# Kernel tuning notes

Hardware: AMD Instinct MI355X
Metric: run time of the kernel (lower is better)

Reference implementation:

```python
import jax, jax.numpy as jnp
from jax import lax
import numpy as np

B, C_IN, H, W = 32, 3, 256, 256
EMB_DIM, NUM_EMB = 64, 512
COMMIT = 0.25
DN = ('NCHW', 'OIHW', 'NCHW')


def conv2d(x, w, b, stride, pad):
    y = lax.conv_general_dilated(x, w, (stride, stride), [(pad, pad), (pad, pad)],
                                 dimension_numbers=DN)
    return y + b[None, :, None, None]


def conv_transpose2d(x, w, b, stride, pad):
    # torch ConvTranspose2d weight layout: (in_ch, out_ch, kh, kw)
    # equivalent: regular conv with spatially flipped, (in,out)-swapped kernel,
    # lhs_dilation=stride, padding = k - 1 - pad on each side.
    k = w.shape[2]
    w_conv = jnp.flip(w, (2, 3)).transpose(1, 0, 2, 3)  # -> OIHW
    p = k - 1 - pad
    y = lax.conv_general_dilated(x, w_conv, (1, 1), [(p, p), (p, p)],
                                 lhs_dilation=(stride, stride), dimension_numbers=DN)
    return y + b[None, :, None, None]


def setup_inputs() -> dict:
    key = jax.random.key(0)
    ks = jax.random.split(key, 8)

    def rn(k, shape):
        fan_in = int(np.prod(shape[1:]))
        return jax.random.normal(k, shape, jnp.float32) / np.float32(np.sqrt(fan_in))

    return {
        "x": jax.random.normal(ks[0], (B, C_IN, H, W), jnp.float32),
        "e1_w": rn(ks[1], (32, C_IN, 4, 4)), "e1_b": jnp.zeros((32,), jnp.float32),
        "e2_w": rn(ks[2], (EMB_DIM, 32, 4, 4)), "e2_b": jnp.zeros((EMB_DIM,), jnp.float32),
        "emb": jax.random.uniform(ks[3], (NUM_EMB, EMB_DIM), jnp.float32,
                                  -1.0 / NUM_EMB, 1.0 / NUM_EMB),
        # decoder ConvTranspose weights in torch (in, out, k, k) layout
        "d1_w": rn(ks[4], (EMB_DIM, 64, 4, 4)), "d1_b": jnp.zeros((64,), jnp.float32),
        "d2_w": rn(ks[5], (64, 32, 4, 4)), "d2_b": jnp.zeros((32,), jnp.float32),
        "d3_w": rn(ks[6], (C_IN, 32, 3, 3)), "d3_b": jnp.zeros((C_IN,), jnp.float32),
    }


def vq(z, emb):
    Bz, Cz, Hz, Wz = z.shape
    flat = z.transpose(0, 2, 3, 1).reshape(-1, Cz)  # (B*H*W, C), NHWC order
    # squared euclidean distances; argmin identical to cdist argmin
    d2 = (jnp.sum(flat * flat, axis=1, keepdims=True)
          - 2.0 * flat @ emb.T
          + jnp.sum(emb * emb, axis=1))  # (N, K)
    idx = jnp.argmin(d2, axis=1)
    q_flat = emb[idx]  # gather == one-hot matmul in original
    # FAITHFUL to torch: .view(x.shape) reinterprets NHWC-ordered rows as NCHW
    quantized = q_flat.reshape(z.shape)
    loss = (COMMIT * jnp.mean((lax.stop_gradient(quantized) - z) ** 2)
            + jnp.mean((quantized - lax.stop_gradient(z)) ** 2))
    q_st = z + lax.stop_gradient(quantized - z)  # straight-through
    return q_st, loss, idx.reshape(Bz, Hz, Wz)


def reference(x, e1_w, e1_b, e2_w, e2_b, emb, d1_w, d1_b, d2_w, d2_b, d3_w, d3_b):
    z = jax.nn.relu(conv2d(x, e1_w, e1_b, 2, 1))
    z = jax.nn.relu(conv2d(z, e2_w, e2_b, 2, 1))
    q_st, vq_loss, _ = vq(z, emb)
    h = jax.nn.relu(conv_transpose2d(q_st, d1_w, d1_b, 2, 1))
    h = jax.nn.relu(conv_transpose2d(h, d2_w, d2_b, 2, 1))
    recon = jax.nn.sigmoid(conv2d(h, d3_w, d3_b, 1, 1))
    return recon, vq_loss, q_st
```

## Files before the change

### kernel.cpp

```cpp
#include <hip/hip_runtime.h>
#include <math.h>

#define BB    32
#define C_IN  3
#define H0    256
#define W0    256
#define C1    32
#define H1    128
#define W1    128
#define C2    64
#define H2    64
#define W2    64
#define HW2   (H2*W2)
#define N_EMB 512
#define E_DIM 64
#define NZ    (BB*C2*HW2)
#define NPX   (BB*HW2)

typedef unsigned short u16;
typedef unsigned int   uint;
typedef __attribute__((ext_vector_type(8))) short short8;
typedef __attribute__((ext_vector_type(4))) float f32x4;

__device__ inline u16 f2bf(float f) {
    uint u = __builtin_bit_cast(uint, f);
    u += 0x7FFF + ((u >> 16) & 1);
    return (u16)(u >> 16);
}
__device__ inline float bf2f(u16 h) {
    uint u = (uint)h << 16;
    return __builtin_bit_cast(float, u);
}
__device__ inline f32x4 mfma16(short8 a, short8 b, f32x4 c) {
    return __builtin_amdgcn_mfma_f32_16x16x32_bf16(a, b, c, 0, 0, 0);
}
template<int RS>
__device__ inline int swz(int off) { return off ^ (((off >> RS) & 7) << 4); }

template<int C, int HP, int WP, int H, int W>
__global__ __launch_bounds__(256) void border_zero(u16* buf, int nimg) {
    int t = blockIdx.x * 256 + threadIdx.x;
    if (t >= nimg * HP * WP) return;
    int x = t % WP, y = (t / WP) % HP;
    if (y >= 1 && y < 1 + H && x >= 1 && x < 1 + W) return;
    uint4 z4; z4.x = 0; z4.y = 0; z4.z = 0; z4.w = 0;
    uint4* p = (uint4*)(buf + (size_t)t * C);
    #pragma unroll
    for (int i = 0; i < C / 8; ++i) p[i] = z4;
}

template<int CI, int CO>
__global__ __launch_bounds__(256) void wt_deconv(const float* __restrict__ w,
        u16* __restrict__ wb) {
    int i = blockIdx.x * 256 + threadIdx.x;
    if (i >= 4 * CO * 4 * CI) return;
    int ic  = i % CI;
    int t   = (i / CI) & 3;
    int oc  = (i / (CI * 4)) % CO;
    int cls = i / (CI * 4 * CO);
    int py = cls >> 1, px = cls & 1, ty = t >> 1, tx = t & 1;
    int ky = py ? (ty ? 0 : 2) : (ty ? 3 : 1);
    int kx = px ? (tx ? 0 : 2) : (tx ? 3 : 1);
    wb[i] = f2bf(w[(((size_t)ic * CO + oc) * 4 + ky) * 4 + kx]);
}

__global__ __launch_bounds__(256) void wt_conv2(const float* __restrict__ w,
        u16* __restrict__ wb) {
    int i = blockIdx.x * 256 + threadIdx.x;
    if (i >= 64 * 512) return;
    int ic = i & 31;
    int k  = (i >> 5) & 15;
    int oc = i >> 9;
    wb[i] = f2bf(w[(size_t)(oc * 32 + ic) * 16 + k]);
}

__global__ __launch_bounds__(256) void wt_conv3(const float* __restrict__ w,
        u16* __restrict__ wk) {
    int i = blockIdx.x * 256 + threadIdx.x;
    if (i >= 16 * 288) return;
    int ic = i & 31;
    int k  = (i / 32) % 9;
    int oc = i / 288;
    float hi = 0.f, lo = 0.f;
    if (oc < 3) {
        float v = w[(size_t)(oc * 32 + ic) * 9 + k];
        hi = bf2f(f2bf(v));
        lo = v - hi;
    }
    wk[i]            = f2bf(hi);
    wk[i + 16 * 288] = f2bf(lo);
}

__global__ __launch_bounds__(256) void wt_emb(const float* __restrict__ emb,
        u16* __restrict__ ehi, u16* __restrict__ elo) {
    int i = blockIdx.x * 256 + threadIdx.x;
    float v = emb[i];
    u16 h = f2bf(v);
    ehi[i] = h;
    elo[i] = f2bf(v - bf2f(h));
}

__global__ __launch_bounds__(256) void conv1_kernel(const float* __restrict__ x,
        const float* __restrict__ w, const float* __restrict__ bias,
        u16* __restrict__ out) {
    int t = blockIdx.x * 256 + threadIdx.x;
    int ox = t & (W1 - 1);
    int oy = (t >> 7) & (H1 - 1);
    int b  = t >> 14;
    const float* xb = x + (size_t)b * (C_IN * H0 * W0);
    float v[48];
    #pragma unroll
    for (int ic = 0; ic < 3; ++ic)
        #pragma unroll
        for (int dy = 0; dy < 4; ++dy) {
            int iy = oy * 2 - 1 + dy;
            #pragma unroll
            for (int dx = 0; dx < 4; ++dx) {
                int ix = ox * 2 - 1 + dx;
                float val = 0.f;
                if ((unsigned)iy < H0 && (unsigned)ix < W0)
                    val = xb[((size_t)ic * H0 + iy) * W0 + ix];
                v[(ic * 4 + dy) * 4 + dx] = val;
            }
        }
    u16 h[32];
    #pragma unroll
    for (int oc = 0; oc < C1; ++oc) {
        float a = bias[oc];
        #pragma unroll
        for (int k = 0; k < 48; ++k) a = fmaf(v[k], w[oc * 48 + k], a);
        h[oc] = f2bf(fmaxf(a, 0.f));
    }
    uint4* dst = (uint4*)(out + ((size_t)(b * 131 + oy + 1) * 131 + ox + 1) * 32);
    #pragma unroll
    for (int i = 0; i < 4; ++i) {
        uint4 u;
        u.x = (uint)h[i*8+0] | ((uint)h[i*8+1] << 16);
        u.y = (uint)h[i*8+2] | ((uint)h[i*8+3] << 16);
        u.z = (uint)h[i*8+4] | ((uint)h[i*8+5] << 16);
        u.w = (uint)h[i*8+6] | ((uint)h[i*8+7] << 16);
        dst[i] = u;
    }
}

__global__ __launch_bounds__(256) void conv2_mfma(const u16* __restrict__ z1p,
        const u16* __restrict__ wb, const float* __restrict__ bias,
        float* __restrict__ z) {
    __shared__ u16 wlds[32 * 512];
    int xcd = blockIdx.x & 7;
    int oh  = (blockIdx.x >> 3) & 1;
    int bx  = (blockIdx.x >> 4) * 8 + xcd;
    for (int j = threadIdx.x; j < 2048; j += 256) {
        int u = j * 8;
        int byteoff = swz<10>(u * 2);
        *(uint4*)((char*)wlds + byteoff) =
            *(const uint4*)(wb + (size_t)(oh * 32) * 512 + u);
    }
    __syncthreads();
    int wid = threadIdx.x >> 6, lane = threadIdx.x & 63;
    int m0 = bx * 128 + wid * 32;
    int b  = m0 >> 12;
    int y  = (m0 >> 6) & 63;
    int x0 = m0 & 63;
    int l15 = lane & 15, lk = lane >> 4;
    f32x4 acc[2][2] = {};
    int xA = x0 + l15, xB = x0 + 16 + l15;
    for (int ks = 0; ks < 16; ++ks) {
        int dy = ks >> 2, dx = ks & 3;
        int rb = (b * 131 + 2 * y + dy) * 131;
        short8 fbA = *(const short8*)(z1p + ((size_t)(rb + 2 * xA + dx)) * 32 + lk * 8);
        short8 fbB = *(const short8*)(z1p + ((size_t)(rb + 2 * xB + dx)) * 32 + lk * 8);
        #pragma unroll
        for (int f = 0; f < 2; ++f) {
            int byteoff = swz<10>((f * 16 + l15) * 1024 + ks * 64 + lk * 16);
            short8 fa = *(const short8*)((const char*)wlds + byteoff);
            acc[0][f] = mfma16(fa, fbA, acc[0][f]);
            acc[1][f] = mfma16(fa, fbB, acc[1][f]);
        }
    }
    #pragma unroll
    for (int p = 0; p < 2; ++p) {
        int pix = m0 + p * 16 + l15;
        #pragma unroll
        for (int f = 0; f < 2; ++f) {
            int oc0 = oh * 32 + f * 16 + lk * 4;
            float4 bi = *(const float4*)(bias + oc0);
            float4 r;
            r.x = fmaxf(acc[p][f][0] + bi.x, 0.f);
            r.y = fmaxf(acc[p][f][1] + bi.y, 0.f);
            r.z = fmaxf(acc[p][f][2] + bi.z, 0.f);
            r.w = fmaxf(acc[p][f][3] + bi.w, 0.f);
            *(float4*)(z + (size_t)pix * 64 + oc0) = r;
        }
    }
}

__global__ void e2_kernel(const float* __restrict__ emb, float* __restrict__ e2) {
    int e = blockIdx.x * 64 + threadIdx.x;
    float s = 0.f;
    #pragma unroll
    for (int c = 0; c < E_DIM; ++c) {
        float v = emb[(size_t)e * E_DIM + c];
        s = fmaf(v, v, s);
    }
    e2[e] = s;
}

__global__ __launch_bounds__(256) void vq_mfma(const float* __restrict__ zf,
        const u16* __restrict__ ehi, const u16* __restrict__ elo,
        const float* __restrict__ e2, const float* __restrict__ emb,
        float* __restrict__ q, u16* __restrict__ dq) {
    int wid = threadIdx.x >> 6, lane = threadIdx.x & 63;
    int l15 = lane & 15, lk = lane >> 4;
    int m0 = (blockIdx.x * 4 + wid) * 32;
    short8 zh[2][2], zl[2][2];
    #pragma unroll
    for (int h = 0; h < 2; ++h) {
        int px = m0 + h * 16 + l15;
        const float4* zp = (const float4*)(zf + (size_t)px * 64);
        #pragma unroll
        for (int ks = 0; ks < 2; ++ks) {
            short8 hh, ll;
            #pragma unroll
            for (int j2 = 0; j2 < 2; ++j2) {
                float4 v4 = zp[ks * 8 + lk * 2 + j2];
                float vv[4] = {v4.x, v4.y, v4.z, v4.w};
                #pragma unroll
                for (int j = 0; j < 4; ++j) {
                    u16 hb = f2bf(vv[j]);
                    hh[j2 * 4 + j] = (short)hb;
                    ll[j2 * 4 + j] = (short)f2bf(vv[j] - bf2f(hb));
                }
            }
            zh[h][ks] = hh;
            zl[h][ks] = ll;
        }
    }
    float bs[2] = {3.4e38f, 3.4e38f};
    int   bi[2] = {0, 0};
    for (int tile = 0; tile < 32; ++tile) {
        short8 fh[2], fl[2];
        #pragma unroll
        for (int ks = 0; ks < 2; ++ks) {
            fh[ks] = *(const short8*)(ehi + (size_t)(tile * 16 + l15) * 64 + ks * 32 + lk * 8);
            fl[ks] = *(const short8*)(elo + (size_t)(tile * 16 + l15) * 64 + ks * 32 + lk * 8);
        }
        float4 e2v = *(const float4*)(e2 + tile * 16 + lk * 4);
        float ee[4] = {e2v.x, e2v.y, e2v.z, e2v.w};
        #pragma unroll
        for (int h = 0; h < 2; ++h) {
            f32x4 acc = {};
            #pragma unroll
            for (int ks = 0; ks < 2; ++ks) {
                acc = mfma16(fh[ks], zh[h][ks], acc);
                acc = mfma16(fl[ks], zh[h][ks], acc);
                acc = mfma16(fh[ks], zl[h][ks], acc);
            }
            #pragma unroll
            for (int r = 0; r < 4; ++r) {
                float sc = ee[r] - 2.f * acc[r];
                int ei = tile * 16 + lk * 4 + r;
                if (sc < bs[h]) { bs[h] = sc; bi[h] = ei; }
            }
        }
    }
    #pragma unroll
    for (int h = 0; h < 2; ++h) {
        #pragma unroll
        for (int off = 16; off < 64; off <<= 1) {
            float s2 = __shfl_xor(bs[h], off, 64);
            int   i2 = __shfl_xor(bi[h], off, 64);
            if (s2 < bs[h] || (s2 == bs[h] && i2 < bi[h])) { bs[h] = s2; bi[h] = i2; }
        }
    }
    #pragma unroll
    for (int h = 0; h < 2; ++h) {
        for (int p = 0; p < 16; ++p) {
            int idx = __shfl(bi[h], p, 64);
            int px  = m0 + h * 16 + p;
            float val = emb[(size_t)idx * 64 + lane];
            q[(size_t)px * 64 + lane] = val;
            int xx = px & 63, yy = (px >> 6) & 63, bb = px >> 12;
            dq[((size_t)(bb * 66 + yy + 1) * 66 + xx + 1) * 64 + lane] = f2bf(val);
        }
    }
}

__global__ __launch_bounds__(256) void loss_tr(const float* __restrict__ q,
        const float* __restrict__ z, float* __restrict__ part) {
    __shared__ float zt[64 * 65];
    int bh = blockIdx.x;
    size_t zbase = (size_t)bh * 4096;
    for (int j = threadIdx.x; j < 4096; j += 256) {
        int w = j >> 6, c = j & 63;
        zt[w * 65 + c] = z[zbase + j];
    }
    __syncthreads();
    int b = bh >> 6, h = bh & 63;
    int w = threadIdx.x & 63;
    float s = 0.f;
    #pragma unroll
    for (int k = 0; k < 16; ++k) {
        int cc = (threadIdx.x >> 6) + k * 4;
        float qv = q[(size_t)b * 262144 + (size_t)cc * 4096 + h * 64 + w];
        float d = qv - zt[w * 65 + cc];
        s = fmaf(d, d, s);
    }
    #pragma unroll
    for (int off = 32; off; off >>= 1) s += __shfl_down(s, off, 64);
    __shared__ float red[4];
    int lane = threadIdx.x & 63, wid = threadIdx.x >> 6;
    if (lane == 0) red[wid] = s;
    __syncthreads();
    if (threadIdx.x == 0) part[blockIdx.x] = (red[0] + red[1]) + (red[2] + red[3]);
}

__global__ __launch_bounds__(256) void loss_final(const float* __restrict__ part,
        float* __restrict__ loss, float scale) {
    float s = 0.f;
    for (int i = threadIdx.x; i < 2048; i += 256) s += part[i];
    #pragma unroll
    for (int off = 32; off; off >>= 1) s += __shfl_down(s, off, 64);
    __shared__ float red[4];
    int lane = threadIdx.x & 63, wid = threadIdx.x >> 6;
    if (lane == 0) red[wid] = s;
    __syncthreads();
    if (threadIdx.x == 0)
        *loss = ((red[0] + red[1]) + (red[2] + red[3])) * scale;
}

template<int CO, int NOC, int PT, int HI, int WI, int NYB>
__global__ __launch_bounds__(256) void deconv_lds(const u16* __restrict__ in,
        const u16* __restrict__ wb, const float* __restrict__ bias,
        u16* __restrict__ out) {
    constexpr int HPI = HI + 2, WPI = WI + 2;
    constexpr int HPO = 2 * HI + 2, WPO = 2 * WI + 2;
    constexpr int NF = NOC / 16;
    constexpr int NW16 = 2 * NOC * 256;
    constexpr int LOG2NYB = (NYB == 4) ? 2 : 1;
    __shared__ u16 wlds[NW16];
    int xcd = blockIdx.x & 7;
    int byv = (blockIdx.x >> 3) & (NYB - 1);
    int bx  = (blockIdx.x >> (3 + LOG2NYB)) * 8 + xcd;
    int py = byv & 1;
    int oh = byv >> 1;
    int oc_base = oh * NOC;
    for (int j = threadIdx.x; j < NW16 / 8; j += 256) {
        int u = j * 8;
        int clsl = u / (NOC * 256);
        int rem = u - clsl * (NOC * 256);
        int byteoff = swz<9>(u * 2);
        *(uint4*)((char*)wlds + byteoff) = *(const uint4*)(wb
            + ((size_t)((py * 2 + clsl) * CO + oc_base)) * 256 + rem);
    }
    __syncthreads();
    int sy = py ? 1 : -1;
    int wid = threadIdx.x >> 6, lane = threadIdx.x & 63;
    int m0 = bx * (PT * 64) + wid * (PT * 16);
    int b = m0 / (HI * WI);
    int rem0 = m0 % (HI * WI);
    int y = rem0 / WI, x0 = rem0 % WI;
    int l15 = lane & 15, lk = lane >> 4;

    short8 fbuf[2][3][2][PT];
    #pragma unroll
    for (int idy = 0; idy < 2; ++idy) {
        int dy = idy ? sy : 0;
        int rb = (b * HPI + y + dy + 1) * WPI;
        #pragma unroll
        for (int idx = 0; idx < 3; ++idx)
            #pragma unroll
            for (int ks = 0; ks < 2; ++ks)
                #pragma unroll
                for (int p = 0; p < PT; ++p)
                    fbuf[idy][idx][ks][p] = *(const short8*)(in
                        + (size_t)(rb + x0 + p * 16 + l15 + idx) * 64
                        + ks * 32 + lk * 8);
    }

    f32x4 acc[PT][2][NF] = {};
    #pragma unroll
    for (int idy = 0; idy < 2; ++idy)
        #pragma unroll
        for (int idx = 0; idx < 3; ++idx) {
            int dx = idx - 1;
            #pragma unroll
            for (int ks = 0; ks < 2; ++ks)
                #pragma unroll
                for (int pxc = 0; pxc < 2; ++pxc) {
                    int sx = pxc ? 1 : -1;
                    if (!(dx == 0 || dx == sx)) continue;
                    int t = 2 * (idy != 0) + (dx != 0);
                    #pragma unroll
                    for (int f = 0; f < NF; ++f) {
                        int row = pxc * NOC + f * 16 + l15;
                        int byteoff = swz<9>(row * 512 + (t * 2 + ks) * 64 + lk * 16);
                        short8 fa = *(const short8*)((const char*)wlds + byteoff);
                        #pragma unroll
                        for (int p = 0; p < PT; ++p)
                            acc[p][pxc][f] = mfma16(fa, fbuf[idy][idx][ks][p],
                                                    acc[p][pxc][f]);
                    }
                }
        }

    #pragma unroll
    for (int p = 0; p < PT; ++p) {
        int x = x0 + p * 16 + l15;
        #pragma unroll
        for (int pxc = 0; pxc < 2; ++pxc) {
            int oy = 2 * y + py + 1, ox = 2 * x + pxc + 1;
            size_t po = ((size_t)(b * HPO + oy) * WPO + ox) * CO;
            #pragma unroll
            for (int f = 0; f < NF; ++f) {
                int oc0 = oc_base + f * 16 + lk * 4;
                float4 bi = *(const float4*)(bias + oc0);
                float r0 = fmaxf(acc[p][pxc][f][0] + bi.x, 0.f);
                float r1 = fmaxf(acc[p][pxc][f][1] + bi.y, 0.f);
                float r2 = fmaxf(acc[p][pxc][f][2] + bi.z, 0.f);
                float r3 = fmaxf(acc[p][pxc][f][3] + bi.w, 0.f);
                uint2 uu;
                uu.x = (uint)f2bf(r0) | ((uint)f2bf(r1) << 16);
                uu.y = (uint)f2bf(r2) | ((uint)f2bf(r3) << 16);
                *(uint2*)(out + po + oc0) = uu;
            }
        }
    }
}

__global__ __launch_bounds__(512) void deconv2_stage(const u16* __restrict__ in,
        const u16* __restrict__ wb, const float* __restrict__ bias,
        u16* __restrict__ out) {
    __shared__ u16 wlds[2 * 32 * 256];
    __shared__ u16 ilds[2 * 130 * 64];
    int xcd = blockIdx.x & 7;
    int py  = (blockIdx.x >> 3) & 1;
    int bx  = (blockIdx.x >> 4) * 8 + xcd;
    int b = bx >> 7;
    int y = bx & 127;
    int sy = py ? 1 : -1;
    for (int j = threadIdx.x; j < 2048; j += 512) {
        int u = j * 8;
        int clsl = u >> 13;
        int rem = u & 8191;
        *(uint4*)((char*)wlds + swz<9>(u * 2)) = *(const uint4*)(wb
            + ((size_t)(py * 2 + clsl) * 32) * 256 + rem);
    }
    int rowg0 = (b * 130 + y + 1) * 130;
    int rowg1 = (b * 130 + y + sy + 1) * 130;
    for (int j = threadIdx.x; j < 2080; j += 512) {
        int row = (j >= 1040);
        int rem = j - row * 1040;
        int px = rem >> 3, c16 = rem & 7;
        int rg = row ? rowg1 : rowg0;
        uint4 v = *(const uint4*)(in + (size_t)(rg + px) * 64 + c16 * 8);
        int lbyte = (j * 16) ^ ((px & 7) << 4);
        *(uint4*)((char*)ilds + lbyte) = v;
    }
    __syncthreads();

    int wid = threadIdx.x >> 6, lane = threadIdx.x & 63;
    int l15 = lane & 15, lk = lane >> 4;
    int xw = wid * 16;
    f32x4 acc[2][2] = {};
    #pragma unroll
    for (int idy = 0; idy < 2; ++idy)
        #pragma unroll
        for (int idx = 0; idx < 3; ++idx) {
            int dx = idx - 1;
            #pragma unroll
            for (int ks = 0; ks < 2; ++ks) {
                int pxl = xw + l15 + idx;
                int lbyte = ((idy * 130 + pxl) * 128 + ks * 64 + lk * 16)
                            ^ ((pxl & 7) << 4);
                short8 fb = *(const short8*)((const char*)ilds + lbyte);
                #pragma unroll
                for (int pxc = 0; pxc < 2; ++pxc) {
                    int sx = pxc ? 1 : -1;
                    if (!(dx == 0 || dx == sx)) continue;
                    int t = 2 * (idy != 0) + (dx != 0);
                    #pragma unroll
                    for (int f = 0; f < 2; ++f) {
                        int row = pxc * 32 + f * 16 + l15;
                        int byteoff = swz<9>(row * 512 + (t * 2 + ks) * 64 + lk * 16);
                        short8 fa = *(const short8*)((const char*)wlds + byteoff);
                        acc[pxc][f] = mfma16(fa, fb, acc[pxc][f]);
                    }
                }
            }
        }

    int x = xw + l15;
    #pragma unroll
    for (int pxc = 0; pxc < 2; ++pxc) {
        int oy = 2 * y + py + 1, ox = 2 * x + pxc + 1;
        size_t po = ((size_t)(b * 258 + oy) * 258 + ox) * 32;
        #pragma unroll
        for (int f = 0; f < 2; ++f) {
            int oc0 = f * 16 + lk * 4;
            float4 bi = *(const float4*)(bias + oc0);
            float r0 = fmaxf(acc[pxc][f][0] + bi.x, 0.f);
            float r1 = fmaxf(acc[pxc][f][1] + bi.y, 0.f);
            float r2 = fmaxf(acc[pxc][f][2] + bi.z, 0.f);
            float r3 = fmaxf(acc[pxc][f][3] + bi.w, 0.f);
            uint2 uu;
            uu.x = (uint)f2bf(r0) | ((uint)f2bf(r1) << 16);
            uu.y = (uint)f2bf(r2) | ((uint)f2bf(r3) << 16);
            *(uint2*)(out + po + oc0) = uu;
        }
    }
}

__global__ __launch_bounds__(256) void conv3_mfma(const u16* __restrict__ in,
        const u16* __restrict__ wk, const float* __restrict__ bias,
        float* __restrict__ out) {
    __shared__ u16 walds[16 * 288 * 2];
    for (int j = threadIdx.x; j < 1152; j += 256) {
        int u = j * 8;
        *(uint4*)((char*)walds + swz<9>(u * 2)) = *(const uint4*)(wk + u);
    }
    __syncthreads();
    int wid = threadIdx.x >> 6, lane = threadIdx.x & 63;
    int m0 = (blockIdx.x * 4 + wid) * 16;
    int b   = m0 >> 16;
    int rem = m0 & 65535;
    int y   = rem >> 8;
    int x0  = rem & 255;
    int l15 = lane & 15, lk = lane >> 4;
    short8 fb[3][3];
    #pragma unroll
    for (int dy = 0; dy < 3; ++dy) {
        int rb = (b * 258 + y + dy) * 258;
        #pragma unroll
        for (int dx = 0; dx < 3; ++dx)
            fb[dy][dx] = *(const short8*)(in + (size_t)(rb + x0 + l15 + dx) * 32 + lk * 8);
    }
    f32x4 acc = {};
    #pragma unroll
    for (int ks = 0; ks < 9; ++ks) {
        int base = (l15 * 288 + ks * 32 + lk * 8) * 2;
        short8 fah = *(const short8*)((const char*)walds + swz<9>(base));
        short8 fal = *(const short8*)((const char*)walds + swz<9>(base + 9216));
        acc = mfma16(fah, fb[ks / 3][ks % 3], acc);
        acc = mfma16(fal, fb[ks / 3][ks % 3], acc);
    }
    if (lk == 0) {
        int px = x0 + l15;
        float* ob = out + (size_t)b * 196608 + (size_t)y * 256 + px;
        ob[0]      = 1.f / (1.f + expf(-(acc[0] + bias[0])));
        ob[65536]  = 1.f / (1.f + expf(-(acc[1] + bias[1])));
        ob[131072] = 1.f / (1.f + expf(-(acc[2] + bias[2])));
    }
}

extern "C" void kernel_launch(void* const* d_in, const int* in_sizes, int n_in,
                              void* d_out, int out_size, void* d_ws, size_t ws_size,
                              hipStream_t stream) {
    (void)in_sizes; (void)n_in; (void)out_size;
    const float* x   = (const float*)d_in[0];
    const float* e1w = (const float*)d_in[1];
    const float* e1b = (const float*)d_in[2];
    const float* e2w = (const float*)d_in[3];
    const float* e2b = (const float*)d_in[4];
    const float* emb = (const float*)d_in[5];
    const float* d1w = (const float*)d_in[6];
    const float* d1b = (const float*)d_in[7];
    const float* d2w = (const float*)d_in[8];
    const float* d2b = (const float*)d_in[9];
    const float* d3w = (const float*)d_in[10];
    const float* d3b = (const float*)d_in[11];

    float* out   = (float*)d_out;
    float* recon = out;
    float* loss  = out + 6291456;
    float* q     = out + 6291457;

    char* wsb = (char*)d_ws;
    u16*   wt1b = (u16*)(wsb + 0);
    u16*   wt2b = (u16*)(wsb + 131072);
    u16*   wc2b = (u16*)(wsb + 196608);
    float* e2v  = (float*)(wsb + 262144);
    float* prt  = (float*)(wsb + 264192);
    u16*   wk3  = (u16*)(wsb + 272384);
    u16*   ehib = (u16*)(wsb + 290816);
    u16*   elob = (u16*)(wsb + 356352);
    char*  big  = wsb + 524288;

    u16*   z1p = (u16*)big;
    float* zf  = (float*)(big + 35145728);
    u16* dq = (u16*)big;

    size_t avail = ws_size > (size_t)524288 ? ws_size - 524288 : 0;
    int G = 32;
    while (G > 1 && (size_t)17842176 + (size_t)G * 6423296 > avail) G >>= 1;
    int ngrp = BB / G;
    u16* h1p = (u16*)(big + 17842176);
    u16* h2p = (u16*)(big + 17842176 + (size_t)G * 2163200);

    wt_deconv<64, 64><<<256, 256, 0, stream>>>(d1w, wt1b);
    wt_deconv<64, 32><<<128, 256, 0, stream>>>(d2w, wt2b);
    wt_conv2<<<128, 256, 0, stream>>>(e2w, wc2b);
    wt_conv3<<<18, 256, 0, stream>>>(d3w, wk3);
    wt_emb<<<128, 256, 0, stream>>>(emb, ehib, elob);
    e2_kernel<<<8, 64, 0, stream>>>(emb, e2v);

    border_zero<32, 131, 131, 128, 128><<<2146, 256, 0, stream>>>(z1p, 32);
    conv1_kernel<<<2048, 256, 0, stream>>>(x, e1w, e1b, z1p);
    conv2_mfma<<<2048, 256, 0, stream>>>(z1p, wc2b, e2b, zf);
    border_zero<64, 66, 66, 64, 64><<<545, 256, 0, stream>>>(dq, 32);
    vq_mfma<<<1024, 256, 0, stream>>>(zf, ehib, elob, e2v, emb, q, dq);
    loss_tr<<<2048, 256, 0, stream>>>(q, zf, prt);

    border_zero<64, 130, 130, 128, 128><<<(G * 16900 + 255) / 256, 256, 0, stream>>>(h1p, G);
    border_zero<32, 258, 258, 256, 256><<<(G * 66564 + 255) / 256, 256, 0, stream>>>(h2p, G);
    for (int g = 0; g < ngrp; ++g) {
        u16* dqg = dq + (size_t)g * G * 278784;
        deconv_lds<64, 32, 2, 64, 64, 4>
            <<<G * 32 * 4, 256, 0, stream>>>(dqg, wt1b, d1b, h1p);
        deconv2_stage<<<G * 128 * 2, 512, 0, stream>>>(h1p, wt2b, d2b, h2p);
        conv3_mfma<<<G * 1024, 256, 0, stream>>>(h2p, wk3, d3b,
                                                 recon + (size_t)g * G * 196608);
    }
    loss_final<<<1, 256, 0, stream>>>(prt, loss, 1.25f / (float)NZ);
}
```

Before: 450.6 us.

## Stage deconv1 input rows in LDS and use 512-thread blocks

Replaces the templated deconv_lds kernel for the first transposed convolution with a dedicated deconv1_stage kernel. Each 512-thread block loads three padded input rows into swizzled LDS alongside the weights, and the waves read their B fragments from LDS instead of each wave issuing its own global loads. This cuts redundant global traffic for the overlapping 3-wide, 2-row neighbourhoods and reduces per-thread register use (one pixel tile instead of two). The cost is extra LDS, a barrier on the input staging, and a different block-to-tile mapping.

```diff
diff --git a/kernel.cpp b/kernel.cpp
--- a/kernel.cpp
+++ b/kernel.cpp
@@ -329,101 +329,90 @@
         *loss = ((red[0] + red[1]) + (red[2] + red[3])) * scale;
 }
 
-template<int CO, int NOC, int PT, int HI, int WI, int NYB>
-__global__ __launch_bounds__(256) void deconv_lds(const u16* __restrict__ in,
+__global__ __launch_bounds__(512) void deconv1_stage(const u16* __restrict__ in,
         const u16* __restrict__ wb, const float* __restrict__ bias,
         u16* __restrict__ out) {
-    constexpr int HPI = HI + 2, WPI = WI + 2;
-    constexpr int HPO = 2 * HI + 2, WPO = 2 * WI + 2;
-    constexpr int NF = NOC / 16;
-    constexpr int NW16 = 2 * NOC * 256;
-    constexpr int LOG2NYB = (NYB == 4) ? 2 : 1;
-    __shared__ u16 wlds[NW16];
+    __shared__ u16 wlds[2 * 32 * 256];
+    __shared__ u16 ilds[3 * 66 * 64];
     int xcd = blockIdx.x & 7;
-    int byv = (blockIdx.x >> 3) & (NYB - 1);
-    int bx  = (blockIdx.x >> (3 + LOG2NYB)) * 8 + xcd;
-    int py = byv & 1;
-    int oh = byv >> 1;
-    int oc_base = oh * NOC;
-    for (int j = threadIdx.x; j < NW16 / 8; j += 256) {
+    int pv  = (blockIdx.x >> 3) & 3;
+    int bx  = (blockIdx.x >> 5) * 8 + xcd;
+    int py = pv & 1;
+    int oh = pv >> 1;
+    int b  = bx >> 5;
+    int y0 = (bx & 31) * 2;
+    for (int j = threadIdx.x; j < 2048; j += 512) {
         int u = j * 8;
-        int clsl = u / (NOC * 256);
-        int rem = u - clsl * (NOC * 256);
-        int byteoff = swz<9>(u * 2);
-        *(uint4*)((char*)wlds + byteoff) = *(const uint4*)(wb
-            + ((size_t)((py * 2 + clsl) * CO + oc_base)) * 256 + rem);
+        int clsl = u >> 13;
+        int rem = u & 8191;
+        *(uint4*)((char*)wlds + swz<9>(u * 2)) = *(const uint4*)(wb
+            + ((size_t)((py * 2 + clsl) * 64 + oh * 32)) * 256 + rem);
+    }
+    int rows_start = y0 - 1 + py;
+    for (int j = threadIdx.x; j < 1584; j += 512) {
+        int rr = j / 528;
+        int rem = j - rr * 528;
+        int px = rem >> 3, c16 = rem & 7;
+        uint4 v = *(const uint4*)(in
+            + ((size_t)(b * 66 + rows_start + 1 + rr) * 66 + px) * 64 + c16 * 8);
+        int lbyte = (j * 16) ^ ((px & 7) << 4);
+        *(uint4*)((char*)ilds + lbyte) = v;
     }
     __syncthreads();
-    int sy = py ? 1 : -1;
+
     int wid = threadIdx.x >> 6, lane = threadIdx.x & 63;
-    int m0 = bx * (PT * 64) + wid * (PT * 16);
-    int b = m0 / (HI * WI);
-    int rem0 = m0 % (HI * WI);
-    int y = rem0 / WI, x0 = rem0 % WI;
     int l15 = lane & 15, lk = lane >> 4;
-
-    short8 fbuf[2][3][2][PT];
+    int pxb = wid * 16;
+    int r   = pxb >> 6;
+    int xw  = pxb & 63;
+    int y   = y0 + r;
+    f32x4 acc[2][2] = {};
     #pragma unroll
     for (int idy = 0; idy < 2; ++idy) {
-        int dy = idy ? sy : 0;
-        int rb = (b * HPI + y + dy + 1) * WPI;
-        #pragma unroll
-        for (int idx = 0; idx < 3; ++idx)
-            #pragma unroll
-            for (int ks = 0; ks < 2; ++ks)
-                #pragma unroll
-                for (int p = 0; p < PT; ++p)
-                    fbuf[idy][idx][ks][p] = *(const short8*)(in
-                        + (size_t)(rb + x0 + p * 16 + l15 + idx) * 64
-                        + ks * 32 + lk * 8);
-    }
-
-    f32x4 acc[PT][2][NF] = {};
-    #pragma unroll
-    for (int idy = 0; idy < 2; ++idy)
+        int rr = r + (idy ? py : (1 - py));
         #pragma unroll
         for (int idx = 0; idx < 3; ++idx) {
             int dx = idx - 1;
             #pragma unroll
-            for (int ks = 0; ks < 2; ++ks)
+            for (int ks = 0; ks < 2; ++ks) {
+                int pxl = xw + l15 + idx;
+                int lbyte = ((rr * 66 + pxl) * 128 + ks * 64 + lk * 16)
+                            ^ ((pxl & 7) << 4);
+                short8 fb = *(const short8*)((const char*)ilds + lbyte);
                 #pragma unroll
                 for (int pxc = 0; pxc < 2; ++pxc) {
                     int sx = pxc ? 1 : -1;
                     if (!(dx == 0 || dx == sx)) continue;
                     int t = 2 * (idy != 0) + (dx != 0);
                     #pragma unroll
-                    for (int f = 0; f < NF; ++f) {
-                        int row = pxc * NOC + f * 16 + l15;
+                    for (int f = 0; f < 2; ++f) {
+                        int row = pxc * 32 + f * 16 + l15;
                         int byteoff = swz<9>(row * 512 + (t * 2 + ks) * 64 + lk * 16);
                         short8 fa = *(const short8*)((const char*)wlds + byteoff);
-                        #pragma unroll
-                        for (int p = 0; p < PT; ++p)
-                            acc[p][pxc][f] = mfma16(fa, fbuf[idy][idx][ks][p],
-                                                    acc[p][pxc][f]);
+                        acc[pxc][f] = mfma16(fa, fb, acc[pxc][f]);
                     }
                 }
-        }
-
-    #pragma unroll
-    for (int p = 0; p < PT; ++p) {
-        int x = x0 + p * 16 + l15;
-        #pragma unroll
-        for (int pxc = 0; pxc < 2; ++pxc) {
-            int oy = 2 * y + py + 1, ox = 2 * x + pxc + 1;
-            size_t po = ((size_t)(b * HPO + oy) * WPO + ox) * CO;
-            #pragma unroll
-            for (int f = 0; f < NF; ++f) {
-                int oc0 = oc_base + f * 16 + lk * 4;
-                float4 bi = *(const float4*)(bias + oc0);
-                float r0 = fmaxf(acc[p][pxc][f][0] + bi.x, 0.f);
-                float r1 = fmaxf(acc[p][pxc][f][1] + bi.y, 0.f);
-                float r2 = fmaxf(acc[p][pxc][f][2] + bi.z, 0.f);
-                float r3 = fmaxf(acc[p][pxc][f][3] + bi.w, 0.f);
-                uint2 uu;
-                uu.x = (uint)f2bf(r0) | ((uint)f2bf(r1) << 16);
-                uu.y = (uint)f2bf(r2) | ((uint)f2bf(r3) << 16);
-                *(uint2*)(out + po + oc0) = uu;
             }
+        }
+    }
+
+    int x = xw + l15;
+    #pragma unroll
+    for (int pxc = 0; pxc < 2; ++pxc) {
+        int oy = 2 * y + py + 1, ox = 2 * x + pxc + 1;
+        size_t po = ((size_t)(b * 130 + oy) * 130 + ox) * 64;
+        #pragma unroll
+        for (int f = 0; f < 2; ++f) {
+            int oc0 = oh * 32 + f * 16 + lk * 4;
+            float4 bi = *(const float4*)(bias + oc0);
+            float r0 = fmaxf(acc[pxc][f][0] + bi.x, 0.f);
+            float r1 = fmaxf(acc[pxc][f][1] + bi.y, 0.f);
+            float r2 = fmaxf(acc[pxc][f][2] + bi.z, 0.f);
+            float r3 = fmaxf(acc[pxc][f][3] + bi.w, 0.f);
+            uint2 uu;
+            uu.x = (uint)f2bf(r0) | ((uint)f2bf(r1) << 16);
+            uu.y = (uint)f2bf(r2) | ((uint)f2bf(r3) << 16);
+            *(uint2*)(out + po + oc0) = uu;
         }
     }
 }
@@ -615,8 +604,7 @@
     border_zero<32, 258, 258, 256, 256><<<(G * 66564 + 255) / 256, 256, 0, stream>>>(h2p, G);
     for (int g = 0; g < ngrp; ++g) {
         u16* dqg = dq + (size_t)g * G * 278784;
-        deconv_lds<64, 32, 2, 64, 64, 4>
-            <<<G * 32 * 4, 256, 0, stream>>>(dqg, wt1b, d1b, h1p);
+        deconv1_stage<<<G * 32 * 4, 512, 0, stream>>>(dqg, wt1b, d1b, h1p);
         deconv2_stage<<<G * 128 * 2, 512, 0, stream>>>(h1p, wt2b, d2b, h2p);
         conv3_mfma<<<G * 1024, 256, 0, stream>>>(h2p, wk3, d3b,
                                                  recon + (size_t)g * G * 196608);
```

Measured after the change: 433.4 us. 1.04x faster.
